# Optimization experiments

Hardware: AMD Instinct MI355X
Metric: run time of the kernel (lower is better)

Reference implementation:

```python
import jax, jax.numpy as jnp
import numpy as np

GROUP_SIZE = 64
OUT_FEATURES = 4096
IN_FEATURES = 4096
NUM_GROUPS = IN_FEATURES // GROUP_SIZE


def setup_inputs() -> dict:
    key = jax.random.key(0)
    k1, k2, k3, k4, k5 = jax.random.split(key, 5)
    x = jax.random.normal(k1, (4, 2048, IN_FEATURES), dtype=jnp.float32)
    # Packed bytes: two 4-bit nibbles per byte (uint8 semantics, stored as int32).
    weight_packed = jax.random.randint(k2, (OUT_FEATURES * NUM_GROUPS, GROUP_SIZE // 2), 0, 256, dtype=jnp.int32)
    # Per-group affine params; small scales keep dequantized weights realistic.
    weight_scales = jax.random.uniform(k3, (OUT_FEATURES * NUM_GROUPS,), dtype=jnp.float32) * 0.01 + 1e-4
    weight_zeros = jax.random.normal(k4, (OUT_FEATURES * NUM_GROUPS,), dtype=jnp.float32) * 0.05
    bias = jax.random.normal(k5, (OUT_FEATURES,), dtype=jnp.float32) * 0.02
    return {"x": x, "weight_packed": weight_packed, "weight_scales": weight_scales,
            "weight_zeros": weight_zeros, "bias": bias}


def _dequantize_4bit(packed, scales, zeros):
    # packed: [G, group_size//2] ints in [0,256). low nibble -> even slots, high -> odd.
    low = (packed & 15).astype(jnp.float32)
    high = ((packed >> 4) & 15).astype(jnp.float32)
    g = packed.shape[0]
    unpacked = jnp.stack([low, high], axis=-1).reshape(g, GROUP_SIZE)  # interleave
    deq = unpacked * scales[:, None] + zeros[:, None]
    return deq.reshape(OUT_FEATURES, IN_FEATURES)


def reference(x, weight_packed, weight_scales, weight_zeros, bias):
    weight = _dequantize_4bit(weight_packed, weight_scales, weight_zeros)  # [O, I]
    # F.linear: x @ weight.T + bias
    out = jnp.einsum('bsi,oi->bso', x, weight) + bias
    return out
```

## Files before the change

### kernel.cpp

```cpp
#include <hip/hip_runtime.h>
#include <hip/hip_bf16.h>


typedef short short8 __attribute__((ext_vector_type(8)));
typedef float float4v __attribute__((ext_vector_type(4)));
typedef int int4v __attribute__((ext_vector_type(4)));

#define M_TOTAL 8192
#define N_OUT 4096
#define K_IN 4096
#define BM 256
#define BN 256
#define BK 64
#define NT (K_IN / BK)

__device__ __forceinline__ short f2bf(float f) {
  unsigned int u = __builtin_bit_cast(unsigned int, f);
  unsigned int r = (u + 0x7fffu + ((u >> 16) & 1u)) >> 16;
  return (short)(unsigned short)r;
}

__device__ __forceinline__ void gload_lds16(const void* g, void* l) {
  __builtin_amdgcn_global_load_lds(
      (const __attribute__((address_space(1))) void*)g,
      (__attribute__((address_space(3))) void*)l, 16, 0, 0);
}

__global__ __launch_bounds__(256)
void cvt_x_kernel(const float* __restrict__ x, short* __restrict__ xb, int n8) {
  int i = blockIdx.x * blockDim.x + threadIdx.x;
  int stride = gridDim.x * blockDim.x;
  for (; i < n8; i += stride) {
    const float* p = x + (size_t)i * 8;
    float4v f0 = *reinterpret_cast<const float4v*>(p);
    float4v f1 = *reinterpret_cast<const float4v*>(p + 4);
    short8 v;
#pragma unroll
    for (int e = 0; e < 4; ++e) { v[e] = f2bf(f0[e]); v[4 + e] = f2bf(f1[e]); }
    *reinterpret_cast<short8*>(xb + (size_t)i * 8) = v;
  }
}

__global__ __launch_bounds__(256)
void deq_w_kernel(const int* __restrict__ wp, const float* __restrict__ wsc,
                  const float* __restrict__ wzr, short* __restrict__ wb) {
  int t = blockIdx.x * blockDim.x + threadIdx.x;
  int g = t >> 1, h = t & 1;
  float s = wsc[g], z = wzr[g];
  const int* p = wp + (size_t)g * 32 + h * 16;
  int4v b[4];
#pragma unroll
  for (int u = 0; u < 4; ++u) b[u] = *reinterpret_cast<const int4v*>(p + u * 4);
  short* o = wb + (size_t)t * 32;
#pragma unroll
  for (int u = 0; u < 4; ++u) {
    short8 v;
#pragma unroll
    for (int e = 0; e < 4; ++e) {
      int bb = b[u][e];
      v[2 * e]     = f2bf((float)(bb & 15) * s + z);
      v[2 * e + 1] = f2bf((float)((bb >> 4) & 15) * s + z);
    }
    *reinterpret_cast<short8*>(o + u * 8) = v;
  }
}


#define MFMA_BF16 __builtin_amdgcn_mfma_f32_16x16x32_bf16
#define BAR() __builtin_amdgcn_s_barrier()
#define PRIO1() __builtin_amdgcn_s_setprio(1)
#define PRIO0() __builtin_amdgcn_s_setprio(0)
#define VMCNT6() asm volatile("s_waitcnt vmcnt(6)" ::: "memory")
#define VMCNT0() asm volatile("s_waitcnt vmcnt(0)" ::: "memory")

__global__ __launch_bounds__(512, 2)
void qgemm8_kernel(const short* __restrict__ A, const short* __restrict__ B,
                   const float* __restrict__ bias, float* __restrict__ out) {
  __shared__ __align__(16) char L[131072];

  const int tid  = threadIdx.x;
  const int lane = tid & 63;
  const int w    = tid >> 6;
  const int wm   = w >> 2;
  const int wn   = w & 3;

  const int m0 = blockIdx.y * BM;
  const int o0 = blockIdx.x * BN;

  const int kslot = (lane & 7) ^ ((lane >> 3) & 7);
  const int R0 = w * 16 + (lane >> 3);
  const int R1 = R0 + 8;
  const short* pA0 = A + (size_t)(m0 + (R0 >> 6) * 128 + (R0 & 63)) * K_IN + kslot * 8;
  const short* pA1 = A + (size_t)(m0 + (R1 >> 6) * 128 + (R1 & 63)) * K_IN + kslot * 8;
  const short* pB0 = B + (size_t)(o0 + (R0 >> 5) * 64 + (R0 & 31)) * K_IN + kslot * 8;
  const short* pB1 = B + (size_t)(o0 + (R1 >> 5) * 64 + (R1 & 31)) * K_IN + kslot * 8;
  const int ldsp0 = w * 2048 + lane * 16;
  const int ldsp1 = ldsp0 + 1024;

#define STAGE_A(buf, mg, t) do { \
    gload_lds16(pA0 + (size_t)(mg) * 64 * K_IN + (t) * 64, &L[(buf) * 65536 + (mg) * 16384 + ldsp0]); \
    gload_lds16(pA1 + (size_t)(mg) * 64 * K_IN + (t) * 64, &L[(buf) * 65536 + (mg) * 16384 + ldsp1]); \
  } while (0)
#define STAGE_B(buf, ng, t) do { \
    gload_lds16(pB0 + (size_t)(ng) * 32 * K_IN + (t) * 64, &L[(buf) * 65536 + 32768 + (ng) * 16384 + ldsp0]); \
    gload_lds16(pB1 + (size_t)(ng) * 32 * K_IN + (t) * 64, &L[(buf) * 65536 + 32768 + (ng) * 16384 + ldsp1]); \
  } while (0)

  const int l15   = lane & 15;
  const int abase = wm * 8192 + l15 * 128;
  const int bbase = 32768 + wn * 4096 + l15 * 128;
  const int sl0 = (((lane >> 4) + 0) ^ (lane & 7)) * 16;
  const int sl1 = (((lane >> 4) + 4) ^ (lane & 7)) * 16;

  short8 a[8], bl[4], br[4];

#define RD_A(buf, mg) do { \
    _Pragma("unroll") for (int mf = 0; mf < 4; ++mf) { \
      a[mf * 2 + 0] = *reinterpret_cast<const short8*>(&L[(buf) * 65536 + (mg) * 16384 + abase + mf * 2048 + sl0]); \
      a[mf * 2 + 1] = *reinterpret_cast<const short8*>(&L[(buf) * 65536 + (mg) * 16384 + abase + mf * 2048 + sl1]); \
    } } while (0)
#define RD_B(dst, buf, ng) do { \
    _Pragma("unroll") for (int nf = 0; nf < 2; ++nf) { \
      dst[nf * 2 + 0] = *reinterpret_cast<const short8*>(&L[(buf) * 65536 + (ng) * 16384 + bbase + nf * 2048 + sl0]); \
      dst[nf * 2 + 1] = *reinterpret_cast<const short8*>(&L[(buf) * 65536 + (ng) * 16384 + bbase + nf * 2048 + sl1]); \
    } } while (0)

  float4v acc[8][4];
#pragma unroll
  for (int i = 0; i < 8; ++i)
#pragma unroll
    for (int j = 0; j < 4; ++j) acc[i][j] = (float4v){0.f, 0.f, 0.f, 0.f};

#define DO_QUAD(mg, ng, bb_) do { \
    _Pragma("unroll") for (int ks = 0; ks < 2; ++ks) \
    _Pragma("unroll") for (int mf = 0; mf < 4; ++mf) \
    _Pragma("unroll") for (int nf = 0; nf < 2; ++nf) \
      acc[(mg) * 4 + mf][(ng) * 2 + nf] = \
        MFMA_BF16(a[mf * 2 + ks], bb_[nf * 2 + ks], acc[(mg) * 4 + mf][(ng) * 2 + nf], 0, 0, 0); \
  } while (0)

  STAGE_A(0, 0, 0); STAGE_B(0, 1, 0); STAGE_B(0, 0, 0); STAGE_A(0, 1, 0);
  STAGE_A(1, 0, 1); STAGE_B(1, 1, 1); STAGE_B(1, 0, 1);
  VMCNT6();
  BAR();

  for (int i = 0; i < NT / 2 - 1; ++i) {
    const int t2 = 2 * i + 2, t3 = 2 * i + 3;
    RD_A(0, 0); RD_B(br, 0, 1);
    STAGE_A(1, 1, t3 - 2);
    BAR(); PRIO1(); DO_QUAD(0, 1, br); PRIO0(); BAR();
    RD_B(bl, 0, 0);
    STAGE_A(0, 0, t2);
    BAR(); PRIO1(); DO_QUAD(0, 0, bl); PRIO0(); BAR();
    RD_A(0, 1);
    STAGE_B(0, 1, t2);
    BAR(); PRIO1(); DO_QUAD(1, 0, bl); PRIO0(); BAR();
    STAGE_B(0, 0, t2);
    VMCNT6();
    BAR(); PRIO1(); DO_QUAD(1, 1, br); PRIO0(); BAR();
    RD_A(1, 0); RD_B(br, 1, 1);
    STAGE_A(0, 1, t2);
    BAR(); PRIO1(); DO_QUAD(0, 1, br); PRIO0(); BAR();
    RD_B(bl, 1, 0);
    STAGE_A(1, 0, t3);
    BAR(); PRIO1(); DO_QUAD(0, 0, bl); PRIO0(); BAR();
    RD_A(1, 1);
    STAGE_B(1, 1, t3);
    BAR(); PRIO1(); DO_QUAD(1, 0, bl); PRIO0(); BAR();
    STAGE_B(1, 0, t3);
    VMCNT6();
    BAR(); PRIO1(); DO_QUAD(1, 1, br); PRIO0(); BAR();
  }

  RD_A(0, 0); RD_B(br, 0, 1);
  STAGE_A(1, 1, 63);
  BAR(); PRIO1(); DO_QUAD(0, 1, br); PRIO0(); BAR();
  RD_B(bl, 0, 0);
  BAR(); PRIO1(); DO_QUAD(0, 0, bl); PRIO0(); BAR();
  RD_A(0, 1);
  BAR(); PRIO1(); DO_QUAD(1, 0, bl); PRIO0(); BAR();
  VMCNT0();
  BAR(); PRIO1(); DO_QUAD(1, 1, br); PRIO0(); BAR();
  RD_A(1, 0); RD_B(br, 1, 1);
  BAR(); PRIO1(); DO_QUAD(0, 1, br); PRIO0(); BAR();
  RD_B(bl, 1, 0);
  BAR(); PRIO1(); DO_QUAD(0, 0, bl); PRIO0(); BAR();
  RD_A(1, 1);
  BAR(); PRIO1(); DO_QUAD(1, 0, bl); PRIO0(); BAR();
  PRIO1(); DO_QUAD(1, 1, br); PRIO0();

#pragma unroll
  for (int nf = 0; nf < 4; ++nf) {
    const int col = o0 + wn * 64 + nf * 16 + l15;
    const float bb = bias[col];
#pragma unroll
    for (int mf = 0; mf < 8; ++mf) {
      const int rowb = m0 + wm * 128 + mf * 16 + (lane >> 4) * 4;
#pragma unroll
      for (int r = 0; r < 4; ++r)
        out[(size_t)(rowb + r) * N_OUT + col] = acc[mf][nf][r] + bb;
    }
  }
}

extern "C" void kernel_launch(void* const* d_in, const int* in_sizes, int n_in,
                              void* d_out, int out_size, void* d_ws, size_t ws_size,
                              hipStream_t stream) {
  const float* x    = (const float*)d_in[0];
  const int* wp     = (const int*)d_in[1];
  const float* wsc  = (const float*)d_in[2];
  const float* wzr  = (const float*)d_in[3];
  const float* bias = (const float*)d_in[4];
  float* out = (float*)d_out;

  const size_t xb_bytes = (size_t)M_TOTAL * K_IN * 2;
  short* xb = (short*)d_ws;
  short* wb = (short*)((char*)d_ws + xb_bytes);

  cvt_x_kernel<<<2048, 256, 0, stream>>>(x, xb, (int)((size_t)M_TOTAL * K_IN / 8));
  deq_w_kernel<<<2048, 256, 0, stream>>>(wp, wsc, wzr, wb);
  dim3 grid(N_OUT / BN, M_TOTAL / BM);
  qgemm8_kernel<<<grid, dim3(512), 0, stream>>>(xb, wb, bias, out);
}
```

Baseline: 275.8 us.

## Make GEMM persistent over two M tiles with XCD-aware mapping and cross-tile prefetch

```diff
diff --git a/kernel.cpp b/kernel.cpp
--- a/kernel.cpp
+++ b/kernel.cpp
@@ -65,13 +65,13 @@
   }
 }
 
-
 #define MFMA_BF16 __builtin_amdgcn_mfma_f32_16x16x32_bf16
 #define BAR() __builtin_amdgcn_s_barrier()
 #define PRIO1() __builtin_amdgcn_s_setprio(1)
 #define PRIO0() __builtin_amdgcn_s_setprio(0)
 #define VMCNT6() asm volatile("s_waitcnt vmcnt(6)" ::: "memory")
 #define VMCNT0() asm volatile("s_waitcnt vmcnt(0)" ::: "memory")
+#define LGKM8() asm volatile("s_waitcnt lgkmcnt(8)")
 
 __global__ __launch_bounds__(512, 2)
 void qgemm8_kernel(const short* __restrict__ A, const short* __restrict__ B,
@@ -84,26 +84,36 @@
   const int wm   = w >> 2;
   const int wn   = w & 3;
 
-  const int m0 = blockIdx.y * BM;
-  const int o0 = blockIdx.x * BN;
+  const int id   = blockIdx.x;
+  const int xcd  = id & 7;
+  const int slot = id >> 3;
+  const int by   = 2 * xcd + (slot >> 4);
+  const int bx   = slot & 15;
+  const int o0   = bx * BN;
+  int m0 = by * BM;
 
   const int kslot = (lane & 7) ^ ((lane >> 3) & 7);
   const int R0 = w * 16 + (lane >> 3);
   const int R1 = R0 + 8;
-  const short* pA0 = A + (size_t)(m0 + (R0 >> 6) * 128 + (R0 & 63)) * K_IN + kslot * 8;
-  const short* pA1 = A + (size_t)(m0 + (R1 >> 6) * 128 + (R1 & 63)) * K_IN + kslot * 8;
+  const int rowA0 = (R0 >> 6) * 128 + (R0 & 63);
+  const int rowA1 = (R1 >> 6) * 128 + (R1 & 63);
   const short* pB0 = B + (size_t)(o0 + (R0 >> 5) * 64 + (R0 & 31)) * K_IN + kslot * 8;
   const short* pB1 = B + (size_t)(o0 + (R1 >> 5) * 64 + (R1 & 31)) * K_IN + kslot * 8;
   const int ldsp0 = w * 2048 + lane * 16;
   const int ldsp1 = ldsp0 + 1024;
 
-#define STAGE_A(buf, mg, t) do { \
-    gload_lds16(pA0 + (size_t)(mg) * 64 * K_IN + (t) * 64, &L[(buf) * 65536 + (mg) * 16384 + ldsp0]); \
-    gload_lds16(pA1 + (size_t)(mg) * 64 * K_IN + (t) * 64, &L[(buf) * 65536 + (mg) * 16384 + ldsp1]); \
+  const short* pA0 = A + (size_t)(m0 + rowA0) * K_IN + kslot * 8;
+  const short* pA1 = A + (size_t)(m0 + rowA1) * K_IN + kslot * 8;
+  const short* qA0 = pA0 + (size_t)4096 * K_IN;
+  const short* qA1 = pA1 + (size_t)4096 * K_IN;
+
+#define SA(p0_, p1_, buf, mg, t) do { \
+    gload_lds16((p0_) + (size_t)(mg) * 64 * K_IN + (size_t)(t) * 64, &L[(buf) * 65536 + (mg) * 16384 + ldsp0]); \
+    gload_lds16((p1_) + (size_t)(mg) * 64 * K_IN + (size_t)(t) * 64, &L[(buf) * 65536 + (mg) * 16384 + ldsp1]); \
   } while (0)
-#define STAGE_B(buf, ng, t) do { \
-    gload_lds16(pB0 + (size_t)(ng) * 32 * K_IN + (t) * 64, &L[(buf) * 65536 + 32768 + (ng) * 16384 + ldsp0]); \
-    gload_lds16(pB1 + (size_t)(ng) * 32 * K_IN + (t) * 64, &L[(buf) * 65536 + 32768 + (ng) * 16384 + ldsp1]); \
+#define SB(buf, ng, t) do { \
+    gload_lds16(pB0 + (size_t)(ng) * 32 * K_IN + (size_t)(t) * 64, &L[(buf) * 65536 + 32768 + (ng) * 16384 + ldsp0]); \
+    gload_lds16(pB1 + (size_t)(ng) * 32 * K_IN + (size_t)(t) * 64, &L[(buf) * 65536 + 32768 + (ng) * 16384 + ldsp1]); \
   } while (0)
 
   const int l15   = lane & 15;
@@ -139,66 +149,110 @@
         MFMA_BF16(a[mf * 2 + ks], bb_[nf * 2 + ks], acc[(mg) * 4 + mf][(ng) * 2 + nf], 0, 0, 0); \
   } while (0)
 
-  STAGE_A(0, 0, 0); STAGE_B(0, 1, 0); STAGE_B(0, 0, 0); STAGE_A(0, 1, 0);
-  STAGE_A(1, 0, 1); STAGE_B(1, 1, 1); STAGE_B(1, 0, 1);
+#define CWRITE(m0_) do { \
+    _Pragma("unroll") for (int nf = 0; nf < 4; ++nf) { \
+      const int col = o0 + wn * 64 + nf * 16 + l15; \
+      const float bb = bias[col]; \
+      _Pragma("unroll") for (int mf = 0; mf < 8; ++mf) { \
+        const int rowb = (m0_) + wm * 128 + mf * 16 + (lane >> 4) * 4; \
+        _Pragma("unroll") for (int r = 0; r < 4; ++r) \
+          __builtin_nontemporal_store(acc[mf][nf][r] + bb, \
+              &out[(size_t)(rowb + r) * N_OUT + col]); \
+      } \
+    } } while (0)
+
+  SA(pA0, pA1, 0, 0, 0); SB(0, 1, 0); SB(0, 0, 0); SA(pA0, pA1, 0, 1, 0);
+  SA(pA0, pA1, 1, 0, 1); SB(1, 1, 1); SB(1, 0, 1);
   VMCNT6();
   BAR();
 
-  for (int i = 0; i < NT / 2 - 1; ++i) {
-    const int t2 = 2 * i + 2, t3 = 2 * i + 3;
-    RD_A(0, 0); RD_B(br, 0, 1);
-    STAGE_A(1, 1, t3 - 2);
-    BAR(); PRIO1(); DO_QUAD(0, 1, br); PRIO0(); BAR();
-    RD_B(bl, 0, 0);
-    STAGE_A(0, 0, t2);
-    BAR(); PRIO1(); DO_QUAD(0, 0, bl); PRIO0(); BAR();
-    RD_A(0, 1);
-    STAGE_B(0, 1, t2);
-    BAR(); PRIO1(); DO_QUAD(1, 0, bl); PRIO0(); BAR();
-    STAGE_B(0, 0, t2);
-    VMCNT6();
-    BAR(); PRIO1(); DO_QUAD(1, 1, br); PRIO0(); BAR();
-    RD_A(1, 0); RD_B(br, 1, 1);
-    STAGE_A(0, 1, t2);
-    BAR(); PRIO1(); DO_QUAD(0, 1, br); PRIO0(); BAR();
-    RD_B(bl, 1, 0);
-    STAGE_A(1, 0, t3);
-    BAR(); PRIO1(); DO_QUAD(0, 0, bl); PRIO0(); BAR();
-    RD_A(1, 1);
-    STAGE_B(1, 1, t3);
-    BAR(); PRIO1(); DO_QUAD(1, 0, bl); PRIO0(); BAR();
-    STAGE_B(1, 0, t3);
-    VMCNT6();
-    BAR(); PRIO1(); DO_QUAD(1, 1, br); PRIO0(); BAR();
-  }
-
-  RD_A(0, 0); RD_B(br, 0, 1);
-  STAGE_A(1, 1, 63);
-  BAR(); PRIO1(); DO_QUAD(0, 1, br); PRIO0(); BAR();
-  RD_B(bl, 0, 0);
-  BAR(); PRIO1(); DO_QUAD(0, 0, bl); PRIO0(); BAR();
-  RD_A(0, 1);
-  BAR(); PRIO1(); DO_QUAD(1, 0, bl); PRIO0(); BAR();
-  VMCNT0();
-  BAR(); PRIO1(); DO_QUAD(1, 1, br); PRIO0(); BAR();
-  RD_A(1, 0); RD_B(br, 1, 1);
-  BAR(); PRIO1(); DO_QUAD(0, 1, br); PRIO0(); BAR();
-  RD_B(bl, 1, 0);
-  BAR(); PRIO1(); DO_QUAD(0, 0, bl); PRIO0(); BAR();
-  RD_A(1, 1);
-  BAR(); PRIO1(); DO_QUAD(1, 0, bl); PRIO0(); BAR();
-  PRIO1(); DO_QUAD(1, 1, br); PRIO0();
-
-#pragma unroll
-  for (int nf = 0; nf < 4; ++nf) {
-    const int col = o0 + wn * 64 + nf * 16 + l15;
-    const float bb = bias[col];
-#pragma unroll
-    for (int mf = 0; mf < 8; ++mf) {
-      const int rowb = m0 + wm * 128 + mf * 16 + (lane >> 4) * 4;
-#pragma unroll
-      for (int r = 0; r < 4; ++r)
-        out[(size_t)(rowb + r) * N_OUT + col] = acc[mf][nf][r] + bb;
+  for (int tile = 0; tile < 2; ++tile) {
+    for (int i = 0; i < NT / 2 - 1; ++i) {
+      const int t2 = 2 * i + 2, t3 = 2 * i + 3;
+      RD_A(0, 0); RD_B(br, 0, 1);
+      SA(pA0, pA1, 1, 1, t3 - 2);
+      LGKM8();
+      BAR(); PRIO1(); DO_QUAD(0, 1, br); PRIO0(); BAR();
+      RD_B(bl, 0, 0);
+      SA(pA0, pA1, 0, 0, t2);
+      BAR(); PRIO1(); DO_QUAD(0, 0, bl); PRIO0(); BAR();
+      RD_A(0, 1);
+      SB(0, 1, t2);
+      BAR(); PRIO1(); DO_QUAD(1, 0, bl); PRIO0(); BAR();
+      SB(0, 0, t2);
+      VMCNT6();
+      BAR(); PRIO1(); DO_QUAD(1, 1, br); PRIO0(); BAR();
+      RD_A(1, 0); RD_B(br, 1, 1);
+      SA(pA0, pA1, 0, 1, t2);
+      LGKM8();
+      BAR(); PRIO1(); DO_QUAD(0, 1, br); PRIO0(); BAR();
+      RD_B(bl, 1, 0);
+      SA(pA0, pA1, 1, 0, t3);
+      BAR(); PRIO1(); DO_QUAD(0, 0, bl); PRIO0(); BAR();
+      RD_A(1, 1);
+      SB(1, 1, t3);
+      BAR(); PRIO1(); DO_QUAD(1, 0, bl); PRIO0(); BAR();
+      SB(1, 0, t3);
+      VMCNT6();
+      BAR(); PRIO1(); DO_QUAD(1, 1, br); PRIO0(); BAR();
+    }
+
+    if (tile == 0) {
+      RD_A(0, 0); RD_B(br, 0, 1);
+      SA(pA0, pA1, 1, 1, 63);
+      LGKM8();
+      BAR(); PRIO1(); DO_QUAD(0, 1, br); PRIO0(); BAR();
+      RD_B(bl, 0, 0);
+      SA(qA0, qA1, 0, 0, 0);
+      BAR(); PRIO1(); DO_QUAD(0, 0, bl); PRIO0(); BAR();
+      RD_A(0, 1);
+      SB(0, 1, 0);
+      BAR(); PRIO1(); DO_QUAD(1, 0, bl); PRIO0(); BAR();
+      SB(0, 0, 0);
+      VMCNT6();
+      BAR(); PRIO1(); DO_QUAD(1, 1, br); PRIO0(); BAR();
+      RD_A(1, 0); RD_B(br, 1, 1);
+      SA(qA0, qA1, 0, 1, 0);
+      LGKM8();
+      BAR(); PRIO1(); DO_QUAD(0, 1, br); PRIO0(); BAR();
+      RD_B(bl, 1, 0);
+      SA(qA0, qA1, 1, 0, 1);
+      BAR(); PRIO1(); DO_QUAD(0, 0, bl); PRIO0(); BAR();
+      RD_A(1, 1);
+      SB(1, 1, 1);
+      BAR(); PRIO1(); DO_QUAD(1, 0, bl); PRIO0(); BAR();
+      SB(1, 0, 1);
+      VMCNT6();
+      BAR(); PRIO1(); DO_QUAD(1, 1, br); PRIO0(); BAR();
+
+      CWRITE(m0);
+#pragma unroll
+      for (int i2 = 0; i2 < 8; ++i2)
+#pragma unroll
+        for (int j2 = 0; j2 < 4; ++j2) acc[i2][j2] = (float4v){0.f, 0.f, 0.f, 0.f};
+      m0 += 4096;
+      pA0 = qA0; pA1 = qA1;
+    } else {
+      RD_A(0, 0); RD_B(br, 0, 1);
+      SA(pA0, pA1, 1, 1, 63);
+      LGKM8();
+      BAR(); PRIO1(); DO_QUAD(0, 1, br); PRIO0(); BAR();
+      RD_B(bl, 0, 0);
+      BAR(); PRIO1(); DO_QUAD(0, 0, bl); PRIO0(); BAR();
+      RD_A(0, 1);
+      BAR(); PRIO1(); DO_QUAD(1, 0, bl); PRIO0(); BAR();
+      VMCNT0();
+      BAR(); PRIO1(); DO_QUAD(1, 1, br); PRIO0(); BAR();
+      RD_A(1, 0); RD_B(br, 1, 1);
+      LGKM8();
+      BAR(); PRIO1(); DO_QUAD(0, 1, br); PRIO0(); BAR();
+      RD_B(bl, 1, 0);
+      BAR(); PRIO1(); DO_QUAD(0, 0, bl); PRIO0(); BAR();
+      RD_A(1, 1);
+      BAR(); PRIO1(); DO_QUAD(1, 0, bl); PRIO0(); BAR();
+      PRIO1(); DO_QUAD(1, 1, br); PRIO0();
+
+      CWRITE(m0);
     }
   }
 }
@@ -219,6 +273,5 @@
 
   cvt_x_kernel<<<2048, 256, 0, stream>>>(x, xb, (int)((size_t)M_TOTAL * K_IN / 8));
   deq_w_kernel<<<2048, 256, 0, stream>>>(wp, wsc, wzr, wb);
-  dim3 grid(N_OUT / BN, M_TOTAL / BM);
-  qgemm8_kernel<<<grid, dim3(512), 0, stream>>>(xb, wb, bias, out);
-}
+  qgemm8_kernel<<<dim3(256), dim3(512), 0, stream>>>(xb, wb, bias, out);
+}
```

After: 385.3 us. 39.7% more time.
